# Optimization experiments

Hardware: AMD Instinct MI355X
Metric: run time of the kernel (lower is better)

The kernel has to match this reference:

```python
import jax, jax.numpy as jnp
import numpy as np
from jax import lax

EPS = 1e-8  # torch CosineSimilarity eps
TAU = 0.5   # temperature

def _l2norm(v):
    # clamp norm like torch.nn.CosineSimilarity
    n = jnp.sqrt(jnp.sum(v * v, axis=-1, keepdims=True))
    return v / jnp.maximum(n, EPS)

def setup_inputs() -> dict:
    key = jax.random.key(0)
    k1, k2, k3, k4 = jax.random.split(key, 4)
    B, C, H, W = 64, 3, 384, 384
    hidden, size, L = 768, 16, 1024
    x = jax.random.normal(k1, (B, C, H, W), dtype=jnp.float32)
    conv_w = jax.random.normal(k2, (hidden, C, size, size), dtype=jnp.float32) * 0.02
    conv_b = jax.random.normal(k3, (hidden,), dtype=jnp.float32) * 0.02
    latent = jax.random.normal(k4, (1, L, hidden), dtype=jnp.float32)
    return {"x": x, "conv_w": conv_w, "conv_b": conv_b, "latent": latent}

def reference(x, conv_w, conv_b, latent):
    B = x.shape[0]
    stride = conv_w.shape[-1]
    # patch embedding: Conv2d stride=kernel (non-overlapping patches)
    patch = lax.conv_general_dilated(
        x, conv_w, window_strides=(stride, stride), padding='VALID',
        dimension_numbers=('NCHW', 'OIHW', 'NCHW')) + conv_b[None, :, None, None]
    D = patch.shape[1]
    patch = patch.reshape(B, D, -1).transpose(0, 2, 1)  # (B, N, D)
    N = patch.shape[1]
    pn = _l2norm(patch)                                  # (B, N, D)
    # all-pairs cosine similarity via GEMM on normalized vectors
    SIM = jnp.einsum('bnd,bmd->bnm', pn, pn)             # (B, N, N)
    off_diag = 1.0 - jnp.eye(N, dtype=SIM.dtype)
    far_sum = jnp.sum(jnp.exp(SIM / TAU) * off_diag, axis=(1, 2))  # (B,)
    # patch vs latent cosine similarity
    ln = _l2norm(latent[0])                              # (L, D)
    close = jnp.einsum('bnd,ld->bnl', pn, ln)            # (B, N, L)
    close_sum = jnp.sum(jnp.exp(close / TAU), axis=(1, 2))  # (B,)
    loss = -jnp.log(close_sum / far_sum)
    return jnp.mean(loss)
```

## Files before the change

kernel.cpp:

```cpp
#include <hip/hip_runtime.h>
#include <hip/hip_bf16.h>
#include <hip/hip_fp8.h>

#define KDIM   768
#define NPATCH 576
#define NPAD   640
#define NBATCH 64
#define MROWS  36864
#define LROWS  1024

typedef __attribute__((ext_vector_type(8))) int int8v;
typedef __attribute__((ext_vector_type(4))) int int4v;
typedef __attribute__((ext_vector_type(4))) float float4v;
typedef unsigned char u8;

__device__ inline u8 f2fp8(float f) { __hip_fp8_e4m3 t(f); return (u8)t.__x; }

__device__ __forceinline__ void gload_lds16(const u8* g, u8* l) {
    __builtin_amdgcn_global_load_lds(
        (const __attribute__((address_space(1))) unsigned int*)g,
        (__attribute__((address_space(3))) unsigned int*)l, 16, 0, 0);
}

__device__ __forceinline__ void ds_read_b256(unsigned addr, int4v& lo, int4v& hi) {
    asm volatile("ds_read_b128 %0, %2\n\tds_read_b128 %1, %2 offset:16"
                 : "=&v"(lo), "=&v"(hi) : "v"(addr));
}

__global__ __launch_bounds__(256) void im2col_cast_v(const float* __restrict__ x,
                                                     u8* __restrict__ A) {
    int t = blockIdx.x * 256 + threadIdx.x;
    int row = t / 48;
    int ci = t - row * 48;
    int c = ci >> 4, i = ci & 15;
    int b = row / NPATCH;
    int p = row - b * NPATCH;
    int ph = p / 24, pw = p - ph * 24;
    const float* src = x + (((size_t)b * 3 + c) * 384 + ph * 16 + i) * 384 + pw * 16;
    float4v f[4];
#pragma unroll
    for (int q = 0; q < 4; q++) f[q] = *(const float4v*)(src + q * 4);
    unsigned int o[4];
#pragma unroll
    for (int q = 0; q < 4; q++) {
        o[q] = 0;
#pragma unroll
        for (int e = 0; e < 4; e++) o[q] |= ((unsigned int)f2fp8(f[q][e])) << (8 * e);
    }
    *(int4v*)(A + (size_t)row * KDIM + c * 256 + i * 16) = *(int4v*)o;
}

__global__ __launch_bounds__(256) void cast_w(const float* __restrict__ src,
                                              u8* __restrict__ dst) {
    int t = blockIdx.x * 256 + threadIdx.x;
    const float* s = src + (size_t)t * 16;
    unsigned int o[4];
#pragma unroll
    for (int q = 0; q < 4; q++) {
        float4v f = *(const float4v*)(s + q * 4);
        o[q] = 0;
#pragma unroll
        for (int e = 0; e < 4; e++) o[q] |= ((unsigned int)f2fp8(f[e] * 32.0f)) << (8 * e);
    }
    *(int4v*)(dst + (size_t)t * 16) = *(int4v*)o;
}

__global__ __launch_bounds__(256) void normalize_latent(const float* __restrict__ src,
                                                        u8* __restrict__ dst) {
    int wave = threadIdx.x >> 6, lane = threadIdx.x & 63;
    int row = blockIdx.x * 4 + wave;
    const float4v* pr = (const float4v*)(src + (size_t)row * KDIM);
    float4v v[3];
    float ss = 0.f;
#pragma unroll
    for (int c = 0; c < 3; c++) {
        v[c] = pr[lane + 64 * c];
#pragma unroll
        for (int e = 0; e < 4; e++) ss += v[c][e] * v[c][e];
    }
#pragma unroll
    for (int off = 32; off; off >>= 1) ss += __shfl_xor(ss, off);
    float scale = 16.0f / fmaxf(sqrtf(ss), 1e-8f);
#pragma unroll
    for (int c = 0; c < 3; c++) {
        unsigned int o = 0;
#pragma unroll
        for (int e = 0; e < 4; e++) o |= ((unsigned int)f2fp8(v[c][e] * scale)) << (8 * e);
        *(unsigned int*)(dst + (size_t)row * KDIM + c * 256 + lane * 4) = o;
    }
}

__global__ __launch_bounds__(256) void inv_norm(const float* __restrict__ rssq,
                                                float* __restrict__ rn) {
    int t = blockIdx.x * 256 + threadIdx.x;
    int p = t % NPAD;
    rn[t] = (p < NPATCH) ? (1.0f / fmaxf(sqrtf(rssq[t]), 1e-8f)) : 0.0f;
}

__device__ __forceinline__ void gemm_mainloop_fp8(const u8* __restrict__ Ab,
                                                  const u8* __restrict__ Bb,
                                                  u8* As, u8* Bs,
                                                  float4v acc[4][4], int sA, int sB) {
    int tid = threadIdx.x;
    int lane = tid & 63;
    int wu = __builtin_amdgcn_readfirstlane(tid >> 6);
    int quad = lane >> 4, l15 = lane & 15;
    int wm = wu & 1, wn = wu >> 1;
    int lr = lane >> 3, ls = lane & 7;
    int gs = ((((ls >> 1) - lr) & 3) << 1) | (ls & 1);
    int gvoff = lr * KDIM + gs * 16;
    const u8* gAu = Ab + (size_t)(wu * 32) * KDIM;
    const u8* gBu = Bb + (size_t)(wu * 32) * KDIM;
    int woffL = wu * 32 * 128;
    int lg = ((quad + (l15 & 3)) & 3) * 32;
    unsigned asb = (unsigned)(size_t)As + (unsigned)((wm * 64 + l15) * 128 + lg);
    unsigned bsb = (unsigned)(size_t)Bs + (unsigned)((wn * 64 + l15) * 128 + lg);

#pragma unroll
    for (int i = 0; i < 4; i++) {
        gload_lds16(gAu + i * 8 * KDIM + gvoff, As + woffL + i * 1024);
        gload_lds16(gBu + i * 8 * KDIM + gvoff, Bs + woffL + i * 1024);
    }
#pragma unroll
    for (int t = 0; t < 6; t++) {
        int cur = (t & 1) * 16384;
        if (t < 5) {
            int nxt = ((t + 1) & 1) * 16384;
            int ks = (t + 1) * 128;
#pragma unroll
            for (int i = 0; i < 4; i++) {
                gload_lds16(gAu + ks + i * 8 * KDIM + gvoff, As + nxt + woffL + i * 1024);
                gload_lds16(gBu + ks + i * 8 * KDIM + gvoff, Bs + nxt + woffL + i * 1024);
            }
            asm volatile("s_waitcnt vmcnt(8)" ::: "memory");
        } else {
            asm volatile("s_waitcnt vmcnt(0)" ::: "memory");
        }
        __builtin_amdgcn_s_barrier();
        asm volatile("" ::: "memory");
        int4v al[4], ah[4], bl[4], bh[4];
#pragma unroll
        for (int i = 0; i < 4; i++) ds_read_b256(asb + cur + i * 2048, al[i], ah[i]);
#pragma unroll
        for (int j = 0; j < 4; j++) ds_read_b256(bsb + cur + j * 2048, bl[j], bh[j]);
        asm volatile("s_waitcnt lgkmcnt(0)"
                     : "+v"(al[0]), "+v"(al[1]), "+v"(al[2]), "+v"(al[3]),
                       "+v"(ah[0]), "+v"(ah[1]), "+v"(ah[2]), "+v"(ah[3]),
                       "+v"(bl[0]), "+v"(bl[1]), "+v"(bl[2]), "+v"(bl[3]),
                       "+v"(bh[0]), "+v"(bh[1]), "+v"(bh[2]), "+v"(bh[3]));
        __builtin_amdgcn_sched_barrier(0);
        int8v a[4], b[4];
#pragma unroll
        for (int i = 0; i < 4; i++)
            a[i] = __builtin_shufflevector(al[i], ah[i], 0, 1, 2, 3, 4, 5, 6, 7);
#pragma unroll
        for (int j = 0; j < 4; j++)
            b[j] = __builtin_shufflevector(bl[j], bh[j], 0, 1, 2, 3, 4, 5, 6, 7);
        __builtin_amdgcn_s_setprio(1);
#pragma unroll
        for (int i = 0; i < 4; i++)
#pragma unroll
            for (int j = 0; j < 4; j++)
                acc[i][j] = __builtin_amdgcn_mfma_scale_f32_16x16x128_f8f6f4(
                    a[i], b[j], acc[i][j], 0, 0, 0, sA, 0, sB);
        __builtin_amdgcn_s_setprio(0);
        asm volatile("" ::: "memory");
        __builtin_amdgcn_s_barrier();
        asm volatile("" ::: "memory");
    }
}

__device__ __forceinline__ float block_reduce_sum(float s, float* red) {
#pragma unroll
    for (int off = 32; off; off >>= 1) s += __shfl_down(s, off);
    int wave = threadIdx.x >> 6, lane = threadIdx.x & 63;
    if (lane == 0) red[wave] = s;
    __syncthreads();
    return red[0] + red[1] + red[2] + red[3];
}

__global__ __launch_bounds__(256) void gemm_conv(const u8* __restrict__ A,
                                                 const u8* __restrict__ Wm,
                                                 const float* __restrict__ bias,
                                                 u8* __restrict__ pn,
                                                 float* __restrict__ rssq) {
    __shared__ u8 As[2 * 128 * 128], Bs[2 * 128 * 128];
    int xcd = blockIdx.x & 7, q = blockIdx.x >> 3;
    int mb = xcd * 36 + q / 6;
    int nb = q % 6;
    int wave = threadIdx.x >> 6, lane = threadIdx.x & 63;
    int quad = lane >> 4, l15 = lane & 15;
    int wm = wave & 1, wn = wave >> 1;
    float4v acc[4][4] = {};
    gemm_mainloop_fp8(A + (size_t)mb * 128 * KDIM, Wm + (size_t)nb * 128 * KDIM,
                      As, Bs, acc, 0x7F7F7F7F, 0x7A7A7A7A);
    float bv[4];
#pragma unroll
    for (int j = 0; j < 4; j++) bv[j] = bias[nb * 128 + wn * 64 + j * 16 + l15];
#pragma unroll
    for (int i = 0; i < 4; i++) {
#pragma unroll
        for (int r = 0; r < 4; r++) {
            int row = mb * 128 + wm * 64 + i * 16 + quad * 4 + r;
            int b = row / NPATCH;
            int prow = row + b * 64;
            float ssq = 0.f;
#pragma unroll
            for (int j = 0; j < 4; j++) {
                int col = nb * 128 + wn * 64 + j * 16 + l15;
                float v = acc[i][j][r] + bv[j];
                ssq += v * v;
                pn[(size_t)prow * KDIM + col] = f2fp8(v * 16.0f);
            }
#pragma unroll
            for (int off = 1; off < 16; off <<= 1) ssq += __shfl_xor(ssq, off);
            if (l15 == 0) atomicAdd(&rssq[prow], ssq);
        }
    }
}

__global__ __launch_bounds__(256) void gemm_sim(const u8* __restrict__ pn,
                                                const float* __restrict__ rn,
                                                float* __restrict__ far_sum) {
    __shared__ u8 As[2 * 128 * 128], Bs[2 * 128 * 128];
    __shared__ float red[4];
    int xcd = blockIdx.x & 7, q = blockIdx.x >> 3;
    int b = xcd * 8 + q / 25;
    int t = q % 25;
    int mt = t / 5, nt = t - mt * 5;
    int wave = threadIdx.x >> 6, lane = threadIdx.x & 63;
    int quad = lane >> 4, l15 = lane & 15;
    int wm = wave & 1, wn = wave >> 1;
    const u8* base = pn + (size_t)b * NPAD * KDIM;
    float4v acc[4][4] = {};
    gemm_mainloop_fp8(base + (size_t)mt * 128 * KDIM, base + (size_t)nt * 128 * KDIM,
                      As, Bs, acc, 0x7B7B7B7B, 0x7B7B7B7B);
    const float* rnb = rn + b * NPAD;
    float rcol[4];
#pragma unroll
    for (int j = 0; j < 4; j++) rcol[j] = rnb[nt * 128 + wn * 64 + j * 16 + l15];
    float s = 0.f;
#pragma unroll
    for (int i = 0; i < 4; i++) {
#pragma unroll
        for (int r = 0; r < 4; r++) {
            int row = mt * 128 + wm * 64 + i * 16 + quad * 4 + r;
            if (row < NPATCH) {
                float rrow = rnb[row];
#pragma unroll
                for (int j = 0; j < 4; j++) {
                    int col = nt * 128 + wn * 64 + j * 16 + l15;
                    if (col < NPATCH && row != col)
                        s += __expf(2.0f * acc[i][j][r] * rrow * rcol[j]);
                }
            }
        }
    }
    float tot = block_reduce_sum(s, red);
    if (threadIdx.x == 0) atomicAdd(&far_sum[b], tot);
}

__global__ __launch_bounds__(256) void gemm_close(const u8* __restrict__ pn,
                                                  const u8* __restrict__ Lm,
                                                  const float* __restrict__ rn,
                                                  float* __restrict__ close_sum) {
    __shared__ u8 As[2 * 128 * 128], Bs[2 * 128 * 128];
    __shared__ float red[4];
    int xcd = blockIdx.x & 7, q = blockIdx.x >> 3;
    int mb = xcd * 40 + (q >> 3);
    int nb = q & 7;
    int wave = threadIdx.x >> 6, lane = threadIdx.x & 63;
    int quad = lane >> 4, l15 = lane & 15;
    int wm = wave & 1, wn = wave >> 1;
    float4v acc[4][4] = {};
    gemm_mainloop_fp8(pn + (size_t)mb * 128 * KDIM, Lm + (size_t)nb * 128 * KDIM,
                      As, Bs, acc, 0x7B7B7B7B, 0x7B7B7B7B);
    int batch = mb / 5;
    int ptile = (mb - batch * 5) * 128;
    float s = 0.f;
#pragma unroll
    for (int i = 0; i < 4; i++) {
#pragma unroll
        for (int r = 0; r < 4; r++) {
            int p = ptile + wm * 64 + i * 16 + quad * 4 + r;
            if (p < NPATCH) {
                float rrow = rn[batch * NPAD + p];
#pragma unroll
                for (int j = 0; j < 4; j++) s += __expf(2.0f * acc[i][j][r] * rrow);
            }
        }
    }
    float tot = block_reduce_sum(s, red);
    if (threadIdx.x == 0) atomicAdd(&close_sum[batch], tot);
}

__global__ void loss_kernel(const float* __restrict__ far_sum,
                            const float* __restrict__ close_sum,
                            float* __restrict__ out) {
    int t = threadIdx.x;
    float v = logf(far_sum[t]) - logf(close_sum[t]);
#pragma unroll
    for (int off = 32; off; off >>= 1) v += __shfl_xor(v, off);
    if (t == 0) out[0] = v * (1.0f / 64.0f);
}

extern "C" void kernel_launch(void* const* d_in, const int* in_sizes, int n_in,
                              void* d_out, int out_size, void* d_ws, size_t ws_size,
                              hipStream_t stream) {
    const float* x      = (const float*)d_in[0];
    const float* conv_w = (const float*)d_in[1];
    const float* conv_b = (const float*)d_in[2];
    const float* latent = (const float*)d_in[3];
    float* out = (float*)d_out;
    char* ws = (char*)d_ws;

    u8* pn = (u8*)ws;
    u8* A  = (u8*)(ws + 31457280);
    u8* Wm = (u8*)(ws + 59768832);
    u8* Lm = (u8*)(ws + 60358656);
    float* rssq = (float*)(ws + 61145088);
    float* sums = (float*)(ws + 61308928);
    float* rn   = (float*)(ws + 31457280);
    float* far_sum = sums;
    float* close_sum = sums + 64;

    hipMemsetAsync(rssq, 0, (40960 + 128) * sizeof(float), stream);
    im2col_cast_v<<<36864 * 48 / 256, 256, 0, stream>>>(x, A);
    cast_w<<<144, 256, 0, stream>>>(conv_w, Wm);
    normalize_latent<<<LROWS / 4, 256, 0, stream>>>(latent, Lm);

    gemm_conv<<<288 * 6, 256, 0, stream>>>(A, Wm, conv_b, pn, rssq);
    inv_norm<<<160, 256, 0, stream>>>(rssq, rn);

    gemm_sim<<<NBATCH * 25, 256, 0, stream>>>(pn, rn, far_sum);
    gemm_close<<<320 * 8, 256, 0, stream>>>(pn, Lm, rn, close_sum);

    loss_kernel<<<1, 64, 0, stream>>>(far_sum, close_sum, out);
}
```

Before: 348.8 us.

## Exploit SIM symmetry, merge sim and close GEMMs, restructure mainloop barriers

```diff
diff --git a/kernel.cpp b/kernel.cpp
--- a/kernel.cpp
+++ b/kernel.cpp
@@ -140,15 +140,17 @@
         asm volatile("" ::: "memory");
         int4v al[4], ah[4], bl[4], bh[4];
 #pragma unroll
+        for (int j = 0; j < 4; j++) ds_read_b256(bsb + cur + j * 2048, bl[j], bh[j]);
+#pragma unroll
         for (int i = 0; i < 4; i++) ds_read_b256(asb + cur + i * 2048, al[i], ah[i]);
-#pragma unroll
-        for (int j = 0; j < 4; j++) ds_read_b256(bsb + cur + j * 2048, bl[j], bh[j]);
         asm volatile("s_waitcnt lgkmcnt(0)"
                      : "+v"(al[0]), "+v"(al[1]), "+v"(al[2]), "+v"(al[3]),
                        "+v"(ah[0]), "+v"(ah[1]), "+v"(ah[2]), "+v"(ah[3]),
                        "+v"(bl[0]), "+v"(bl[1]), "+v"(bl[2]), "+v"(bl[3]),
                        "+v"(bh[0]), "+v"(bh[1]), "+v"(bh[2]), "+v"(bh[3]));
         __builtin_amdgcn_sched_barrier(0);
+        __builtin_amdgcn_s_barrier();
+        asm volatile("" ::: "memory");
         int8v a[4], b[4];
 #pragma unroll
         for (int i = 0; i < 4; i++)
@@ -164,9 +166,6 @@
                 acc[i][j] = __builtin_amdgcn_mfma_scale_f32_16x16x128_f8f6f4(
                     a[i], b[j], acc[i][j], 0, 0, 0, sA, 0, sB);
         __builtin_amdgcn_s_setprio(0);
-        asm volatile("" ::: "memory");
-        __builtin_amdgcn_s_barrier();
-        asm volatile("" ::: "memory");
     }
 }
 
@@ -219,79 +218,81 @@
     }
 }
 
-__global__ __launch_bounds__(256) void gemm_sim(const u8* __restrict__ pn,
-                                                const float* __restrict__ rn,
-                                                float* __restrict__ far_sum) {
+__global__ __launch_bounds__(256) void gemm_scores(const u8* __restrict__ pn,
+                                                   const u8* __restrict__ Lm,
+                                                   const float* __restrict__ rn,
+                                                   float* __restrict__ far_sum,
+                                                   float* __restrict__ close_sum) {
     __shared__ u8 As[2 * 128 * 128], Bs[2 * 128 * 128];
     __shared__ float red[4];
-    int xcd = blockIdx.x & 7, q = blockIdx.x >> 3;
-    int b = xcd * 8 + q / 25;
-    int t = q % 25;
-    int mt = t / 5, nt = t - mt * 5;
-    int wave = threadIdx.x >> 6, lane = threadIdx.x & 63;
-    int quad = lane >> 4, l15 = lane & 15;
-    int wm = wave & 1, wn = wave >> 1;
-    const u8* base = pn + (size_t)b * NPAD * KDIM;
-    float4v acc[4][4] = {};
-    gemm_mainloop_fp8(base + (size_t)mt * 128 * KDIM, base + (size_t)nt * 128 * KDIM,
-                      As, Bs, acc, 0x7B7B7B7B, 0x7B7B7B7B);
-    const float* rnb = rn + b * NPAD;
-    float rcol[4];
-#pragma unroll
-    for (int j = 0; j < 4; j++) rcol[j] = rnb[nt * 128 + wn * 64 + j * 16 + l15];
-    float s = 0.f;
-#pragma unroll
-    for (int i = 0; i < 4; i++) {
-#pragma unroll
-        for (int r = 0; r < 4; r++) {
-            int row = mt * 128 + wm * 64 + i * 16 + quad * 4 + r;
-            if (row < NPATCH) {
-                float rrow = rnb[row];
-#pragma unroll
-                for (int j = 0; j < 4; j++) {
-                    int col = nt * 128 + wn * 64 + j * 16 + l15;
-                    if (col < NPATCH && row != col)
-                        s += __expf(2.0f * acc[i][j][r] * rrow * rcol[j]);
-                }
-            }
-        }
-    }
-    float tot = block_reduce_sum(s, red);
-    if (threadIdx.x == 0) atomicAdd(&far_sum[b], tot);
-}
-
-__global__ __launch_bounds__(256) void gemm_close(const u8* __restrict__ pn,
-                                                  const u8* __restrict__ Lm,
-                                                  const float* __restrict__ rn,
-                                                  float* __restrict__ close_sum) {
-    __shared__ u8 As[2 * 128 * 128], Bs[2 * 128 * 128];
-    __shared__ float red[4];
-    int xcd = blockIdx.x & 7, q = blockIdx.x >> 3;
-    int mb = xcd * 40 + (q >> 3);
-    int nb = q & 7;
     int wave = threadIdx.x >> 6, lane = threadIdx.x & 63;
     int quad = lane >> 4, l15 = lane & 15;
     int wm = wave & 1, wn = wave >> 1;
     float4v acc[4][4] = {};
-    gemm_mainloop_fp8(pn + (size_t)mb * 128 * KDIM, Lm + (size_t)nb * 128 * KDIM,
-                      As, Bs, acc, 0x7B7B7B7B, 0x7B7B7B7B);
-    int batch = mb / 5;
-    int ptile = (mb - batch * 5) * 128;
-    float s = 0.f;
-#pragma unroll
-    for (int i = 0; i < 4; i++) {
-#pragma unroll
-        for (int r = 0; r < 4; r++) {
-            int p = ptile + wm * 64 + i * 16 + quad * 4 + r;
-            if (p < NPATCH) {
-                float rrow = rn[batch * NPAD + p];
-#pragma unroll
-                for (int j = 0; j < 4; j++) s += __expf(2.0f * acc[i][j][r] * rrow);
+
+    if (blockIdx.x < 2560) {
+        int xcd = blockIdx.x & 7, q = blockIdx.x >> 3;
+        int mb = xcd * 40 + (q >> 3);
+        int nb = q & 7;
+        gemm_mainloop_fp8(pn + (size_t)mb * 128 * KDIM, Lm + (size_t)nb * 128 * KDIM,
+                          As, Bs, acc, 0x7B7B7B7B, 0x7B7B7B7B);
+        int batch = mb / 5;
+        int ptile = (mb - batch * 5) * 128;
+        float s = 0.f;
+#pragma unroll
+        for (int i = 0; i < 4; i++) {
+#pragma unroll
+            for (int r = 0; r < 4; r++) {
+                int p = ptile + wm * 64 + i * 16 + quad * 4 + r;
+                if (p < NPATCH) {
+                    float rrow = rn[batch * NPAD + p];
+#pragma unroll
+                    for (int j = 0; j < 4; j++) s += __expf(2.0f * acc[i][j][r] * rrow);
+                }
             }
         }
-    }
-    float tot = block_reduce_sum(s, red);
-    if (threadIdx.x == 0) atomicAdd(&close_sum[batch], tot);
+        float tot = block_reduce_sum(s, red);
+        if (threadIdx.x == 0) atomicAdd(&close_sum[batch], tot);
+    } else {
+        int sbid = blockIdx.x - 2560;
+        int xcd = sbid & 7, q = sbid >> 3;
+        int b = xcd * 8 + q / 15;
+        int t = q % 15;
+        int mt, nt;
+        if (t < 5) { mt = t; nt = t; }
+        else {
+            int u = t - 5;
+            mt = (u < 4) ? 0 : (u < 7) ? 1 : (u < 9) ? 2 : 3;
+            nt = (u < 4) ? u + 1 : (u < 7) ? u - 2 : (u < 9) ? u - 5 : 4;
+        }
+        const u8* base = pn + (size_t)b * NPAD * KDIM;
+        gemm_mainloop_fp8(base + (size_t)mt * 128 * KDIM, base + (size_t)nt * 128 * KDIM,
+                          As, Bs, acc, 0x7B7B7B7B, 0x7B7B7B7B);
+        const float* rnb = rn + b * NPAD;
+        float rcol[4];
+#pragma unroll
+        for (int j = 0; j < 4; j++) rcol[j] = rnb[nt * 128 + wn * 64 + j * 16 + l15];
+        float s = 0.f;
+#pragma unroll
+        for (int i = 0; i < 4; i++) {
+#pragma unroll
+            for (int r = 0; r < 4; r++) {
+                int row = mt * 128 + wm * 64 + i * 16 + quad * 4 + r;
+                if (row < NPATCH) {
+                    float rrow = rnb[row];
+#pragma unroll
+                    for (int j = 0; j < 4; j++) {
+                        int col = nt * 128 + wn * 64 + j * 16 + l15;
+                        if (col < NPATCH && row != col)
+                            s += __expf(2.0f * acc[i][j][r] * rrow * rcol[j]);
+                    }
+                }
+            }
+        }
+        if (mt != nt) s *= 2.0f;
+        float tot = block_reduce_sum(s, red);
+        if (threadIdx.x == 0) atomicAdd(&far_sum[b], tot);
+    }
 }
 
 __global__ void loss_kernel(const float* __restrict__ far_sum,
@@ -332,8 +333,7 @@
     gemm_conv<<<288 * 6, 256, 0, stream>>>(A, Wm, conv_b, pn, rssq);
     inv_norm<<<160, 256, 0, stream>>>(rssq, rn);
 
-    gemm_sim<<<NBATCH * 25, 256, 0, stream>>>(pn, rn, far_sum);
-    gemm_close<<<320 * 8, 256, 0, stream>>>(pn, Lm, rn, close_sum);
+    gemm_scores<<<2560 + 960, 256, 0, stream>>>(pn, Lm, rn, far_sum, close_sum);
 
     loss_kernel<<<1, 64, 0, stream>>>(far_sum, close_sum, out);
 }
```

Measured after the change: 346.5 us. About the same (-0.7%).
